# Performance work log

Measured on AMD Instinct MI355X. Metric: run time of the kernel, lower is better.

The kernel has to match this reference:

```python
import jax, jax.numpy as jnp
import numpy as np

N = 26  # theta length; phi has 2**N = 67,108,864 elements


def setup_inputs() -> dict:
    key = jax.random.key(0)
    k1, k2 = jax.random.split(key)
    theta = jax.random.normal(k1, (N,), dtype=jnp.float32)
    lam = jax.random.normal(k2, (2 ** N,), dtype=jnp.float32)
    return {"theta": theta, "lam": lam}


def reference(theta, lam):
    # phi = kron(v_0, v_1, ..., v_{N-1}) with v_i = [sin|theta_i|, cos|theta_i|]
    # (einsum 'a,b,c,...' followed by flatten == sequential Kronecker product,
    #  with theta[0] mapping to the most-significant bit of the flat index)
    a = jnp.abs(theta)
    vecs = jnp.stack([jnp.sin(a), jnp.cos(a)], axis=1)  # [N, 2]
    phi = vecs[0]
    for i in range(1, N):  # fixed small loop over N factors, not a data dim
        phi = (phi[:, None] * vecs[i][None, :]).reshape(-1)
    # loss = sum(abs(phi - lam)**2); all quantities real
    return jnp.sum(jnp.square(phi - lam))
```

## Files before the change

### kernel.cpp

```cpp
#include <hip/hip_runtime.h>

#define NBITS    26
#define LO_BITS  9
#define MID_BITS 9
#define HI_BITS  8
#define NBLOCKS  2048
#define NTHREADS 256

__global__ __launch_bounds__(NTHREADS) void phi_loss_kernel(
    const float* __restrict__ theta,
    const float* __restrict__ lam,
    float* __restrict__ partial,
    int n4)
{
    __shared__ float s[NBITS], c[NBITS];
    __shared__ float hiT[1 << HI_BITS];
    __shared__ float red[4];

    const int tid = threadIdx.x;

    if (tid < NBITS) {
        float a = fabsf(theta[tid]);
        float sv, cv;
        sincosf(a, &sv, &cv);
        s[tid] = sv;
        c[tid] = cv;
    }
    __syncthreads();

    {
        float p = 1.0f;
        #pragma unroll
        for (int t = 0; t < HI_BITS; ++t)
            p *= ((tid >> t) & 1) ? c[7 - t] : s[7 - t];
        hiT[tid] = p;
    }

    const int S = NBLOCKS * NTHREADS;
    int idx = blockIdx.x * NTHREADS + tid;
    int j = idx << 2;
    int mm = (j >> LO_BITS) & ((1 << MID_BITS) - 1);
    float p = 1.0f;
    #pragma unroll
    for (int t = 0; t < MID_BITS; ++t)
        p *= ((mm >> t) & 1) ? c[16 - t] : s[16 - t];
    int lo = j & ((1 << LO_BITS) - 1);
    #pragma unroll
    for (int t = 2; t < LO_BITS; ++t)
        p *= ((lo >> t) & 1) ? c[25 - t] : s[25 - t];
    float4 mlv;
    mlv.x = p * s[25] * s[24];
    mlv.y = p * c[25] * s[24];
    mlv.z = p * s[25] * c[24];
    mlv.w = p * c[25] * c[24];
    int hidx = j >> (LO_BITS + MID_BITS);
    __syncthreads();

    const float4* __restrict__ lam4 = (const float4*)lam;
    float acc = 0.0f;
    int i4 = idx;
    for (; i4 + 3 * S < n4; i4 += 4 * S, hidx += 32) {
        float4 l0 = lam4[i4];
        float4 l1 = lam4[i4 + S];
        float4 l2 = lam4[i4 + 2 * S];
        float4 l3 = lam4[i4 + 3 * S];
        float h0 = hiT[hidx];
        float h1 = hiT[hidx + 8];
        float h2 = hiT[hidx + 16];
        float h3 = hiT[hidx + 24];
        float d0 = fmaf(h0, mlv.x, -l0.x), d1 = fmaf(h0, mlv.y, -l0.y);
        float d2 = fmaf(h0, mlv.z, -l0.z), d3 = fmaf(h0, mlv.w, -l0.w);
        acc = fmaf(d0, d0, acc); acc = fmaf(d1, d1, acc);
        acc = fmaf(d2, d2, acc); acc = fmaf(d3, d3, acc);
        d0 = fmaf(h1, mlv.x, -l1.x); d1 = fmaf(h1, mlv.y, -l1.y);
        d2 = fmaf(h1, mlv.z, -l1.z); d3 = fmaf(h1, mlv.w, -l1.w);
        acc = fmaf(d0, d0, acc); acc = fmaf(d1, d1, acc);
        acc = fmaf(d2, d2, acc); acc = fmaf(d3, d3, acc);
        d0 = fmaf(h2, mlv.x, -l2.x); d1 = fmaf(h2, mlv.y, -l2.y);
        d2 = fmaf(h2, mlv.z, -l2.z); d3 = fmaf(h2, mlv.w, -l2.w);
        acc = fmaf(d0, d0, acc); acc = fmaf(d1, d1, acc);
        acc = fmaf(d2, d2, acc); acc = fmaf(d3, d3, acc);
        d0 = fmaf(h3, mlv.x, -l3.x); d1 = fmaf(h3, mlv.y, -l3.y);
        d2 = fmaf(h3, mlv.z, -l3.z); d3 = fmaf(h3, mlv.w, -l3.w);
        acc = fmaf(d0, d0, acc); acc = fmaf(d1, d1, acc);
        acc = fmaf(d2, d2, acc); acc = fmaf(d3, d3, acc);
    }
    for (; i4 < n4; i4 += S, hidx += 8) {
        float4 l0 = lam4[i4];
        float h0 = hiT[hidx & ((1 << HI_BITS) - 1)];
        float d0 = fmaf(h0, mlv.x, -l0.x), d1 = fmaf(h0, mlv.y, -l0.y);
        float d2 = fmaf(h0, mlv.z, -l0.z), d3 = fmaf(h0, mlv.w, -l0.w);
        acc = fmaf(d0, d0, acc); acc = fmaf(d1, d1, acc);
        acc = fmaf(d2, d2, acc); acc = fmaf(d3, d3, acc);
    }

    #pragma unroll
    for (int off = 32; off > 0; off >>= 1)
        acc += __shfl_down(acc, off, 64);
    if ((tid & 63) == 0) red[tid >> 6] = acc;
    __syncthreads();
    if (tid == 0)
        partial[blockIdx.x] = (red[0] + red[1]) + (red[2] + red[3]);
}

__global__ __launch_bounds__(64) void finish_kernel(
    const float* __restrict__ partial, float* __restrict__ out)
{
    const int tid = threadIdx.x;
    float acc = 0.0f;
    #pragma unroll
    for (int k = 0; k < NBLOCKS / 64; ++k)
        acc += partial[tid + k * 64];
    #pragma unroll
    for (int off = 32; off > 0; off >>= 1)
        acc += __shfl_down(acc, off, 64);
    if (tid == 0)
        out[0] = acc;
}

extern "C" void kernel_launch(void* const* d_in, const int* in_sizes, int n_in,
                              void* d_out, int out_size, void* d_ws, size_t ws_size,
                              hipStream_t stream) {
    const float* theta = (const float*)d_in[0];
    const float* lam   = (const float*)d_in[1];
    float* out = (float*)d_out;
    float* partial = (float*)d_ws;

    const int n4 = in_sizes[1] >> 2;
    phi_loss_kernel<<<NBLOCKS, NTHREADS, 0, stream>>>(theta, lam, partial, n4);
    finish_kernel<<<1, 64, 0, stream>>>(partial, out);
}
```

Baseline: 51.11 us.

## Give each block a contiguous lam chunk with fixed high bits and precomputed mid table

Each block now handles a contiguous 32K-element slice of lam, so the top 8 bits are fixed per block. The block folds that high product into a 512-entry shared table of mid-bit products. Each thread owns 8 consecutive low-bit factors and loads two float4s per row, which replaces the grid-stride loop over the whole array. The finish kernel also reads partials as float4. Memory access changes from strided to contiguous per block, but the size is now hardcoded to 2^26, the n4 bound is dropped, and each thread issues more loads per iteration.

```diff
diff --git a/kernel.cpp b/kernel.cpp
--- a/kernel.cpp
+++ b/kernel.cpp
@@ -10,14 +10,14 @@
 __global__ __launch_bounds__(NTHREADS) void phi_loss_kernel(
     const float* __restrict__ theta,
     const float* __restrict__ lam,
-    float* __restrict__ partial,
-    int n4)
+    float* __restrict__ partial)
 {
     __shared__ float s[NBITS], c[NBITS];
-    __shared__ float hiT[1 << HI_BITS];
+    __shared__ float mhT[1 << MID_BITS];
     __shared__ float red[4];
 
     const int tid = threadIdx.x;
+    const int b   = blockIdx.x;
 
     if (tid < NBITS) {
         float a = fabsf(theta[tid]);
@@ -28,70 +28,69 @@
     }
     __syncthreads();
 
-    {
-        float p = 1.0f;
+    const int hb = b >> 3;
+    float hprod = 1.0f;
+    #pragma unroll
+    for (int t = 0; t < HI_BITS; ++t)
+        hprod *= ((hb >> t) & 1) ? c[7 - t] : s[7 - t];
+
+    #pragma unroll
+    for (int m = tid; m < (1 << MID_BITS); m += NTHREADS) {
+        float p = hprod;
         #pragma unroll
-        for (int t = 0; t < HI_BITS; ++t)
-            p *= ((tid >> t) & 1) ? c[7 - t] : s[7 - t];
-        hiT[tid] = p;
+        for (int t = 0; t < MID_BITS; ++t)
+            p *= ((m >> t) & 1) ? c[16 - t] : s[16 - t];
+        mhT[m] = p;
     }
 
-    const int S = NBLOCKS * NTHREADS;
-    int idx = blockIdx.x * NTHREADS + tid;
-    int j = idx << 2;
-    int mm = (j >> LO_BITS) & ((1 << MID_BITS) - 1);
-    float p = 1.0f;
+    const int lo0 = (tid & 63) << 3;
+    float p3 = 1.0f;
     #pragma unroll
-    for (int t = 0; t < MID_BITS; ++t)
-        p *= ((mm >> t) & 1) ? c[16 - t] : s[16 - t];
-    int lo = j & ((1 << LO_BITS) - 1);
-    #pragma unroll
-    for (int t = 2; t < LO_BITS; ++t)
-        p *= ((lo >> t) & 1) ? c[25 - t] : s[25 - t];
-    float4 mlv;
-    mlv.x = p * s[25] * s[24];
-    mlv.y = p * c[25] * s[24];
-    mlv.z = p * s[25] * c[24];
-    mlv.w = p * c[25] * c[24];
-    int hidx = j >> (LO_BITS + MID_BITS);
+    for (int t = 3; t < LO_BITS; ++t)
+        p3 *= ((lo0 >> t) & 1) ? c[25 - t] : s[25 - t];
+    float mlv[8];
+    {
+        float s25 = s[25], c25 = c[25], s24 = s[24], c24 = c[24];
+        float a23s = p3 * s[23], a23c = p3 * c[23];
+        mlv[0] = a23s * s24 * s25;  mlv[1] = a23s * s24 * c25;
+        mlv[2] = a23s * c24 * s25;  mlv[3] = a23s * c24 * c25;
+        mlv[4] = a23c * s24 * s25;  mlv[5] = a23c * s24 * c25;
+        mlv[6] = a23c * c24 * s25;  mlv[7] = a23c * c24 * c25;
+    }
     __syncthreads();
 
-    const float4* __restrict__ lam4 = (const float4*)lam;
+    const float4* __restrict__ p4 =
+        (const float4*)lam + ((size_t)b << 13) + (tid << 1);
+    int mm = ((b & 7) << 6) + ((tid >> 6) & 3);
+
     float acc = 0.0f;
-    int i4 = idx;
-    for (; i4 + 3 * S < n4; i4 += 4 * S, hidx += 32) {
-        float4 l0 = lam4[i4];
-        float4 l1 = lam4[i4 + S];
-        float4 l2 = lam4[i4 + 2 * S];
-        float4 l3 = lam4[i4 + 3 * S];
-        float h0 = hiT[hidx];
-        float h1 = hiT[hidx + 8];
-        float h2 = hiT[hidx + 16];
-        float h3 = hiT[hidx + 24];
-        float d0 = fmaf(h0, mlv.x, -l0.x), d1 = fmaf(h0, mlv.y, -l0.y);
-        float d2 = fmaf(h0, mlv.z, -l0.z), d3 = fmaf(h0, mlv.w, -l0.w);
-        acc = fmaf(d0, d0, acc); acc = fmaf(d1, d1, acc);
-        acc = fmaf(d2, d2, acc); acc = fmaf(d3, d3, acc);
-        d0 = fmaf(h1, mlv.x, -l1.x); d1 = fmaf(h1, mlv.y, -l1.y);
-        d2 = fmaf(h1, mlv.z, -l1.z); d3 = fmaf(h1, mlv.w, -l1.w);
-        acc = fmaf(d0, d0, acc); acc = fmaf(d1, d1, acc);
-        acc = fmaf(d2, d2, acc); acc = fmaf(d3, d3, acc);
-        d0 = fmaf(h2, mlv.x, -l2.x); d1 = fmaf(h2, mlv.y, -l2.y);
-        d2 = fmaf(h2, mlv.z, -l2.z); d3 = fmaf(h2, mlv.w, -l2.w);
-        acc = fmaf(d0, d0, acc); acc = fmaf(d1, d1, acc);
-        acc = fmaf(d2, d2, acc); acc = fmaf(d3, d3, acc);
-        d0 = fmaf(h3, mlv.x, -l3.x); d1 = fmaf(h3, mlv.y, -l3.y);
-        d2 = fmaf(h3, mlv.z, -l3.z); d3 = fmaf(h3, mlv.w, -l3.w);
-        acc = fmaf(d0, d0, acc); acc = fmaf(d1, d1, acc);
-        acc = fmaf(d2, d2, acc); acc = fmaf(d3, d3, acc);
-    }
-    for (; i4 < n4; i4 += S, hidx += 8) {
-        float4 l0 = lam4[i4];
-        float h0 = hiT[hidx & ((1 << HI_BITS) - 1)];
-        float d0 = fmaf(h0, mlv.x, -l0.x), d1 = fmaf(h0, mlv.y, -l0.y);
-        float d2 = fmaf(h0, mlv.z, -l0.z), d3 = fmaf(h0, mlv.w, -l0.w);
-        acc = fmaf(d0, d0, acc); acc = fmaf(d1, d1, acc);
-        acc = fmaf(d2, d2, acc); acc = fmaf(d3, d3, acc);
+    #pragma unroll
+    for (int it = 0; it < 16; it += 2) {
+        float4 a0 = p4[0];
+        float4 a1 = p4[1];
+        float4 b0 = p4[512];
+        float4 b1 = p4[513];
+        float pa = mhT[mm];
+        float pb = mhT[mm + 4];
+        float d;
+        d = fmaf(pa, mlv[0], -a0.x); acc = fmaf(d, d, acc);
+        d = fmaf(pa, mlv[1], -a0.y); acc = fmaf(d, d, acc);
+        d = fmaf(pa, mlv[2], -a0.z); acc = fmaf(d, d, acc);
+        d = fmaf(pa, mlv[3], -a0.w); acc = fmaf(d, d, acc);
+        d = fmaf(pa, mlv[4], -a1.x); acc = fmaf(d, d, acc);
+        d = fmaf(pa, mlv[5], -a1.y); acc = fmaf(d, d, acc);
+        d = fmaf(pa, mlv[6], -a1.z); acc = fmaf(d, d, acc);
+        d = fmaf(pa, mlv[7], -a1.w); acc = fmaf(d, d, acc);
+        d = fmaf(pb, mlv[0], -b0.x); acc = fmaf(d, d, acc);
+        d = fmaf(pb, mlv[1], -b0.y); acc = fmaf(d, d, acc);
+        d = fmaf(pb, mlv[2], -b0.z); acc = fmaf(d, d, acc);
+        d = fmaf(pb, mlv[3], -b0.w); acc = fmaf(d, d, acc);
+        d = fmaf(pb, mlv[4], -b1.x); acc = fmaf(d, d, acc);
+        d = fmaf(pb, mlv[5], -b1.y); acc = fmaf(d, d, acc);
+        d = fmaf(pb, mlv[6], -b1.z); acc = fmaf(d, d, acc);
+        d = fmaf(pb, mlv[7], -b1.w); acc = fmaf(d, d, acc);
+        p4 += 1024;
+        mm += 8;
     }
 
     #pragma unroll
@@ -100,17 +99,20 @@
     if ((tid & 63) == 0) red[tid >> 6] = acc;
     __syncthreads();
     if (tid == 0)
-        partial[blockIdx.x] = (red[0] + red[1]) + (red[2] + red[3]);
+        partial[b] = (red[0] + red[1]) + (red[2] + red[3]);
 }
 
 __global__ __launch_bounds__(64) void finish_kernel(
     const float* __restrict__ partial, float* __restrict__ out)
 {
     const int tid = threadIdx.x;
+    const float4* p4 = (const float4*)partial;
     float acc = 0.0f;
     #pragma unroll
-    for (int k = 0; k < NBLOCKS / 64; ++k)
-        acc += partial[tid + k * 64];
+    for (int k = 0; k < NBLOCKS / 4 / 64; ++k) {
+        float4 v = p4[tid + k * 64];
+        acc += (v.x + v.y) + (v.z + v.w);
+    }
     #pragma unroll
     for (int off = 32; off > 0; off >>= 1)
         acc += __shfl_down(acc, off, 64);
@@ -126,7 +128,6 @@
     float* out = (float*)d_out;
     float* partial = (float*)d_ws;
 
-    const int n4 = in_sizes[1] >> 2;
-    phi_loss_kernel<<<NBLOCKS, NTHREADS, 0, stream>>>(theta, lam, partial, n4);
+    phi_loss_kernel<<<NBLOCKS, NTHREADS, 0, stream>>>(theta, lam, partial);
     finish_kernel<<<1, 64, 0, stream>>>(partial, out);
 }
```

Measured after the change: 45.81 us. 1.12x faster.
